# Kernel tuning notes

Measured on AMD Instinct MI355X. Metric: run time of the kernel, lower is better.

## Reference

```python
import jax, jax.numpy as jnp
import numpy as np
from jax import lax

# ---- quantum-kernel constants: flipped model f = Tr[rho(theta) O(patch)] ----
# rho(theta) = (I + sum_i theta_i P_i)/4 over the 15 non-identity 2-qubit Paulis.
# O(patch)  = (M + M^T)/2 where M is the 3x3 patch zero-padded to 16 and reshaped 4x4.
# Both are linear in their inputs, so precompute A[i,k] = Re Tr[P_i O(e_k)] and
# t0[k] = Tr[O(e_k)] once on the host.

def _pauli_features():
    I = np.eye(2, dtype=np.complex64)
    X = np.array([[0, 1], [1, 0]], np.complex64)
    Y = np.array([[0, -1j], [1j, 0]], np.complex64)
    Z = np.array([[1, 0], [0, -1]], np.complex64)
    singles = [I, X, Y, Z]
    paulis = [np.kron(a, b) for a in singles for b in singles][1:]  # 15 non-identity
    A = np.zeros((15, 9), np.float32)
    t0 = np.zeros((9,), np.float32)
    for k in range(9):
        M = np.zeros((4, 4), np.complex64)
        M.flat[k] = 1.0
        O = (M + M.conj().T) / 2.0
        t0[k] = float(np.real(np.trace(O)))
        for i, P in enumerate(paulis):
            A[i, k] = float(np.real(np.trace(P @ O)))
    return A, t0

_A_NP, _T0_NP = _pauli_features()
STRIDE = 1
PAD = (1, 1)  # (pad_h, pad_w)


def setup_inputs() -> dict:
    key = jax.random.key(0)
    k1, k2, k3 = jax.random.split(key, 3)
    x = jax.random.normal(k1, (32, 16, 128, 128), dtype=jnp.float32)
    weight = jax.random.normal(k2, (64, 16, 15), dtype=jnp.float32)
    bias = jax.random.normal(k3, (64, 1), dtype=jnp.float32)
    return {"x": x, "weight": weight, "bias": bias}


def reference(x, weight, bias):
    B, C, H, W = x.shape
    ph, pw = PAD
    Ho = (H - 3 + 2 * ph) // STRIDE + 1
    Wo = (W - 3 + 2 * pw) // STRIDE + 1
    # im2col: [B, C*9, Ho, Wo], channel-major (C slowest, 3x3 row-major fastest)
    patches = lax.conv_general_dilated_patches(
        x, (3, 3), (STRIDE, STRIDE), ((ph, ph), (pw, pw)))
    patches = patches.reshape(B, C, 9, Ho * Wo)  # [B, C, 9, P]

    A = jnp.asarray(_A_NP)    # [15, 9]
    t0 = jnp.asarray(_T0_NP)  # [9]

    # identity part of rho: sum over in-channels of Tr[O]/4 (weight-independent)
    base = jnp.einsum('k,bckp->bp', t0, patches)            # [B, P]
    # Pauli features Tr[P_i O(patch)] per (channel, patch)
    qf = jnp.einsum('ik,bckp->bcip', A, patches)            # [B, C, 15, P]
    out = (base[:, None, :] + jnp.einsum('oci,bcip->bop', weight, qf)) * 0.25
    out = out + bias                                        # bias [O,1] -> [B,O,P]
    return out.reshape(B, weight.shape[0], Ho, Wo)
```

## Files before the change

### kernel.cpp

```cpp
#include <hip/hip_runtime.h>
#include <hip/hip_bf16.h>


typedef short bf16x8 __attribute__((ext_vector_type(8)));
typedef float f32x4 __attribute__((ext_vector_type(4)));

__device__ __forceinline__ void pauli_entry(int s, int r, int c, float& re, float& im) {
    re = 0.f; im = 0.f;
    if (s == 0)      { if (r == c) re = 1.f; }
    else if (s == 1) { if (r != c) re = 1.f; }
    else if (s == 2) { if (r == 0 && c == 1) im = -1.f; else if (r == 1 && c == 0) im = 1.f; }
    else             { if (r == c) re = (r == 0) ? 1.f : -1.f; }
}

__device__ __forceinline__ float A_entry(int i, int k) {
    int j = i + 1, sa = j >> 2, sb = j & 3;
    int r = k >> 2, c = k & 3;
    float ar, ai, br, bi;
    pauli_entry(sa, r >> 1, c >> 1, ar, ai);
    pauli_entry(sb, r & 1, c & 1, br, bi);
    float re1 = ar * br - ai * bi;
    pauli_entry(sa, c >> 1, r >> 1, ar, ai);
    pauli_entry(sb, c & 1, r & 1, br, bi);
    float re2 = ar * br - ai * bi;
    return 0.5f * (re1 + re2);
}

__device__ __forceinline__ short f2bf(float f) {
    union { float f; unsigned int u; } a; a.f = f;
    unsigned int r = a.u + 0x7fffu + ((a.u >> 16) & 1u);
    return (short)(r >> 16);
}

__device__ __forceinline__ unsigned pk_bf16(float a, float b) {
#if __has_builtin(__builtin_amdgcn_cvt_pk_bf16_f32)
    typedef __bf16 bf2 __attribute__((ext_vector_type(2)));
    bf2 r = __builtin_amdgcn_cvt_pk_bf16_f32(a, b);
    union { bf2 v; unsigned u; } cv; cv.v = r;
    return cv.u;
#else
    union { float f; unsigned u; } x, y; x.f = a; y.f = b;
    unsigned ra = x.u + 0x7fffu + ((x.u >> 16) & 1u);
    unsigned rb = y.u + 0x7fffu + ((y.u >> 16) & 1u);
    return (ra >> 16) | (rb & 0xffff0000u);
#endif
}

__global__ __launch_bounds__(256) void prep_kernel(const float* __restrict__ weight,
                                                   short* __restrict__ bfrag) {
    __shared__ float Ash[135];
    int tid = threadIdx.x;
    if (tid < 135) Ash[tid] = A_entry(tid / 9, tid % 9);
    __syncthreads();

    int t = blockIdx.x * 256 + tid;
    if (t >= 1280) return;
    int lane  = t & 63;
    int ot    = (t >> 6) & 3;
    int chunk = t >> 8;
    int q     = lane >> 4;
    int o     = ot * 16 + (lane & 15);
    short vals[8];
    #pragma unroll
    for (int j = 0; j < 8; ++j) {
        int gk = chunk * 32 + q * 8 + j;
        float v = 0.f;
        if (gk < 144) {
            int tap = gk >> 4;
            int c   = gk & 15;
            float acc = (tap == 0 || tap == 5) ? 1.f : 0.f;
            const float* w = weight + (o * 16 + c) * 15;
            #pragma unroll
            for (int i = 0; i < 15; ++i) acc += w[i] * Ash[i * 9 + tap];
            v = 0.25f * acc;
        }
        vals[j] = f2bf(v);
    }
    *(bf16x8*)(bfrag + t * 8) = *(bf16x8*)vals;
}

__global__ __launch_bounds__(256) void conv_mfma(const float* __restrict__ x,
                                                 const short* __restrict__ bfrag,
                                                 const float* __restrict__ bias,
                                                 float* __restrict__ out) {
    __shared__ short sx[10 * 136 * 16];
    __shared__ __align__(16) float obuf[8192];

    const int tid  = threadIdx.x;
    const int h0   = blockIdx.x * 8;
    const int b    = blockIdx.y;
    const int lane = tid & 63;
    const int wave = tid >> 6;
    const int q    = lane >> 4;
    const int nlo  = lane & 15;
    const int otp  = wave >> 1;
    const int hh   = wave & 1;

    const float* xb = x + (size_t)b * 16 * 128 * 128;
    #pragma unroll
    for (int it = 0; it < 11; ++it) {
        int pos = tid + it * 256;
        if (pos < 2720) {
            int seg = pos / 136;
            int w   = pos - seg * 136;
            int row = seg >> 1, chalf = seg & 1;
            int hp  = h0 - 1 + row;
            int xw  = w - 4;
            bool ok = ((unsigned)hp < 128u) && ((unsigned)xw < 128u);
            const float* src = xb + (size_t)(chalf * 8) * 16384 + hp * 128 + xw;
            float v[8];
            #pragma unroll
            for (int j = 0; j < 8; ++j)
                v[j] = ok ? src[(size_t)j * 16384] : 0.f;
            int slot = (chalf ^ (w >> 2)) & 1;
            unsigned* dst = (unsigned*)sx + (row * 136 + w) * 8 + slot * 4;
            #pragma unroll
            for (int j2 = 0; j2 < 4; ++j2)
                dst[j2] = pk_bf16(v[2 * j2], v[2 * j2 + 1]);
        }
    }

    bf16x8 Breg[10];
    #pragma unroll
    for (int ch = 0; ch < 5; ++ch)
        #pragma unroll
        for (int j = 0; j < 2; ++j)
            Breg[ch * 2 + j] = *(const bf16x8*)(bfrag + ((ch * 4 + otp * 2 + j) * 64 + lane) * 8);
    float bv[2];
    #pragma unroll
    for (int j = 0; j < 2; ++j) bv[j] = bias[(otp * 2 + j) * 16 + nlo];

    int baseA[5];
    #pragma unroll
    for (int ch = 0; ch < 5; ++ch) {
        int tap = ch * 2 + (q >> 1);
        if (tap > 8) tap = 8;
        int kh = tap / 3, kw = tap - 3 * kh;
        int chalf = q & 1;
        int row0  = hh * 4 + kh;
        int w0    = nlo + kw + 3;
        int slot  = (chalf ^ (w0 >> 2)) & 1;
        baseA[ch] = (row0 * 136 + w0) * 16 + slot * 8;
    }
    __syncthreads();

    #pragma unroll
    for (int r = 0; r < 4; ++r) {
        const int h = h0 + hh * 4 + r;
        f32x4 acc[2][4][2];
        #pragma unroll
        for (int j = 0; j < 2; ++j)
            #pragma unroll
            for (int np = 0; np < 4; ++np) {
                f32x4 ini = { bv[j], bv[j], bv[j], bv[j] };
                acc[j][np][0] = ini;
                acc[j][np][1] = ini;
            }
        #pragma unroll
        for (int np = 0; np < 4; ++np) {
            #pragma unroll
            for (int ch = 0; ch < 5; ++ch) {
                const short* pA = sx + baseA[ch] + r * 2176 + np * 512;
                bf16x8 A0 = *(const bf16x8*)(pA);
                bf16x8 A1 = *(const bf16x8*)(pA + 256);
                #pragma unroll
                for (int j = 0; j < 2; ++j) {
                    acc[j][np][0] = __builtin_amdgcn_mfma_f32_16x16x32_bf16(A0, Breg[ch * 2 + j], acc[j][np][0], 0, 0, 0);
                    acc[j][np][1] = __builtin_amdgcn_mfma_f32_16x16x32_bf16(A1, Breg[ch * 2 + j], acc[j][np][1], 0, 0, 0);
                }
            }
        }
        #pragma unroll
        for (int j = 0; j < 2; ++j) {
            #pragma unroll
            for (int np = 0; np < 4; ++np)
                #pragma unroll
                for (int mt = 0; mt < 2; ++mt) {
                    int px  = np * 32 + mt * 16 + q * 4;
                    int idx = wave * 2048 + nlo * 128 + (px ^ ((nlo & 7) << 2));
                    *(f32x4*)(obuf + idx) = acc[j][np][mt];
                }
            float* outp = out + (((size_t)b * 64 + (otp * 2 + j) * 16) * 128 + h) * 128;
            #pragma unroll
            for (int i = 0; i < 8; ++i) {
                int o   = 2 * i + (lane >> 5);
                int px  = (lane & 31) * 4;
                int ridx = wave * 2048 + o * 128 + (px ^ ((o & 7) << 2));
                f32x4 v = *(const f32x4*)(obuf + ridx);
                *(f32x4*)(outp + (size_t)o * 16384 + px) = v;
            }
        }
    }
}

extern "C" void kernel_launch(void* const* d_in, const int* in_sizes, int n_in,
                              void* d_out, int out_size, void* d_ws, size_t ws_size,
                              hipStream_t stream) {
    const float* x      = (const float*)d_in[0];
    const float* weight = (const float*)d_in[1];
    const float* bias   = (const float*)d_in[2];
    float* out   = (float*)d_out;
    short* bfrag = (short*)d_ws;

    prep_kernel<<<5, 256, 0, stream>>>(weight, bfrag);
    dim3 grid(16, 32);
    conv_mfma<<<grid, 256, 0, stream>>>(x, bfrag, bias, out);
}
```

Baseline: 169.5 us.

## Halve rows per block, drop LDS output staging, store MFMA results directly

Each block now covers 4 output rows instead of 8, so the grid doubles to 1024 blocks, and the input tile in shared memory shrinks. The 32KB obuf used to stage and transpose outputs is gone. Accumulators are now written straight to global memory as 16-byte stores per lane. A smaller accumulator set and a launch_bounds minimum of 4 blocks aim for higher occupancy. The trade-offs are more redundant halo loads (6 input rows per 4 output rows instead of 10 per 8) and less coalesced global stores, since each lane writes 64B runs across different channels.

```diff
diff --git a/kernel.cpp b/kernel.cpp
--- a/kernel.cpp
+++ b/kernel.cpp
@@ -79,28 +79,27 @@
     *(bf16x8*)(bfrag + t * 8) = *(bf16x8*)vals;
 }
 
-__global__ __launch_bounds__(256) void conv_mfma(const float* __restrict__ x,
-                                                 const short* __restrict__ bfrag,
-                                                 const float* __restrict__ bias,
-                                                 float* __restrict__ out) {
-    __shared__ short sx[10 * 136 * 16];
-    __shared__ __align__(16) float obuf[8192];
+__global__ __launch_bounds__(256, 4) void conv_mfma(const float* __restrict__ x,
+                                                    const short* __restrict__ bfrag,
+                                                    const float* __restrict__ bias,
+                                                    float* __restrict__ out) {
+    __shared__ short sx[6 * 136 * 16];
 
     const int tid  = threadIdx.x;
-    const int h0   = blockIdx.x * 8;
+    const int h0   = blockIdx.x * 4;
     const int b    = blockIdx.y;
     const int lane = tid & 63;
     const int wave = tid >> 6;
     const int q    = lane >> 4;
     const int nlo  = lane & 15;
     const int otp  = wave >> 1;
-    const int hh   = wave & 1;
+    const int rh   = wave & 1;
 
     const float* xb = x + (size_t)b * 16 * 128 * 128;
     #pragma unroll
-    for (int it = 0; it < 11; ++it) {
+    for (int it = 0; it < 7; ++it) {
         int pos = tid + it * 256;
-        if (pos < 2720) {
+        if (pos < 1632) {
             int seg = pos / 136;
             int w   = pos - seg * 136;
             int row = seg >> 1, chalf = seg & 1;
@@ -137,7 +136,7 @@
         if (tap > 8) tap = 8;
         int kh = tap / 3, kw = tap - 3 * kh;
         int chalf = q & 1;
-        int row0  = hh * 4 + kh;
+        int row0  = rh * 2 + kh;
         int w0    = nlo + kw + 3;
         int slot  = (chalf ^ (w0 >> 2)) & 1;
         baseA[ch] = (row0 * 136 + w0) * 16 + slot * 8;
@@ -145,19 +144,17 @@
     __syncthreads();
 
     #pragma unroll
-    for (int r = 0; r < 4; ++r) {
-        const int h = h0 + hh * 4 + r;
-        f32x4 acc[2][4][2];
-        #pragma unroll
-        for (int j = 0; j < 2; ++j)
-            #pragma unroll
-            for (int np = 0; np < 4; ++np) {
-                f32x4 ini = { bv[j], bv[j], bv[j], bv[j] };
-                acc[j][np][0] = ini;
-                acc[j][np][1] = ini;
-            }
+    for (int r = 0; r < 2; ++r) {
+        const int h = h0 + rh * 2 + r;
         #pragma unroll
         for (int np = 0; np < 4; ++np) {
+            f32x4 acc[2][2];
+            #pragma unroll
+            for (int j = 0; j < 2; ++j) {
+                f32x4 ini = { bv[j], bv[j], bv[j], bv[j] };
+                acc[j][0] = ini;
+                acc[j][1] = ini;
+            }
             #pragma unroll
             for (int ch = 0; ch < 5; ++ch) {
                 const short* pA = sx + baseA[ch] + r * 2176 + np * 512;
@@ -165,29 +162,16 @@
                 bf16x8 A1 = *(const bf16x8*)(pA + 256);
                 #pragma unroll
                 for (int j = 0; j < 2; ++j) {
-                    acc[j][np][0] = __builtin_amdgcn_mfma_f32_16x16x32_bf16(A0, Breg[ch * 2 + j], acc[j][np][0], 0, 0, 0);
-                    acc[j][np][1] = __builtin_amdgcn_mfma_f32_16x16x32_bf16(A1, Breg[ch * 2 + j], acc[j][np][1], 0, 0, 0);
+                    acc[j][0] = __builtin_amdgcn_mfma_f32_16x16x32_bf16(A0, Breg[ch * 2 + j], acc[j][0], 0, 0, 0);
+                    acc[j][1] = __builtin_amdgcn_mfma_f32_16x16x32_bf16(A1, Breg[ch * 2 + j], acc[j][1], 0, 0, 0);
                 }
             }
-        }
-        #pragma unroll
-        for (int j = 0; j < 2; ++j) {
             #pragma unroll
-            for (int np = 0; np < 4; ++np)
-                #pragma unroll
-                for (int mt = 0; mt < 2; ++mt) {
-                    int px  = np * 32 + mt * 16 + q * 4;
-                    int idx = wave * 2048 + nlo * 128 + (px ^ ((nlo & 7) << 2));
-                    *(f32x4*)(obuf + idx) = acc[j][np][mt];
-                }
-            float* outp = out + (((size_t)b * 64 + (otp * 2 + j) * 16) * 128 + h) * 128;
-            #pragma unroll
-            for (int i = 0; i < 8; ++i) {
-                int o   = 2 * i + (lane >> 5);
-                int px  = (lane & 31) * 4;
-                int ridx = wave * 2048 + o * 128 + (px ^ ((o & 7) << 2));
-                f32x4 v = *(const f32x4*)(obuf + ridx);
-                *(f32x4*)(outp + (size_t)o * 16384 + px) = v;
+            for (int j = 0; j < 2; ++j) {
+                float* dst = out + (((size_t)b * 64 + (otp * 2 + j) * 16 + nlo) * 128 + h) * 128
+                           + np * 32 + q * 4;
+                *(f32x4*)dst        = acc[j][0];
+                *(f32x4*)(dst + 16) = acc[j][1];
             }
         }
     }
@@ -203,6 +187,6 @@
     short* bfrag = (short*)d_ws;
 
     prep_kernel<<<5, 256, 0, stream>>>(weight, bfrag);
-    dim3 grid(16, 32);
+    dim3 grid(32, 32);
     conv_mfma<<<grid, 256, 0, stream>>>(x, bfrag, bias, out);
 }
```

Result: no change. 166.9 us (-1.5%).
